# Optimization experiments

Measured on AMD Instinct MI355X. Metric: run time of the kernel, lower is better.

## Reference

```python
import jax, jax.numpy as jnp
import numpy as np

B, N, F_IN, F_OUT, H = 8, 1024, 128, 128, 8
D_K = F_OUT // H
NEG = -1.0e9


def setup_inputs() -> dict:
    key = jax.random.key(0)
    ks = jax.random.split(key, 10)
    X = jax.random.normal(ks[0], (B, N, F_IN), dtype=jnp.float32)
    A = (jax.random.uniform(ks[1], (B, N, N)) < 0.1).astype(jnp.float32)
    A = jnp.maximum(A, jnp.eye(N, dtype=jnp.float32)[None])
    s_in = 1.0 / np.sqrt(F_IN)
    s_out = 1.0 / np.sqrt(F_OUT)
    Wq = jax.random.uniform(ks[2], (F_OUT, F_IN), minval=-s_in, maxval=s_in)
    bq = jax.random.uniform(ks[3], (F_OUT,), minval=-s_in, maxval=s_in)
    Wk = jax.random.uniform(ks[4], (F_OUT, F_IN), minval=-s_in, maxval=s_in)
    bk = jax.random.uniform(ks[5], (F_OUT,), minval=-s_in, maxval=s_in)
    Wv = jax.random.uniform(ks[6], (F_OUT, F_IN), minval=-s_in, maxval=s_in)
    bv = jax.random.uniform(ks[7], (F_OUT,), minval=-s_in, maxval=s_in)
    Wo = jax.random.uniform(ks[8], (F_OUT, F_OUT), minval=-s_out, maxval=s_out)
    bo = jax.random.uniform(ks[9], (F_OUT,), minval=-s_out, maxval=s_out)
    return {"X": X, "A": A, "Wq": Wq, "bq": bq, "Wk": Wk, "bk": bk,
            "Wv": Wv, "bv": bv, "Wo": Wo, "bo": bo}


def reference(X, A, Wq, bq, Wk, bk, Wv, bv, Wo, bo):
    # QKV projections (nn.Linear: x @ W.T + b), split into heads
    Q = (X @ Wq.T + bq).reshape(B, N, H, D_K).transpose(0, 2, 1, 3)  # [B,H,N,d]
    K = (X @ Wk.T + bk).reshape(B, N, H, D_K).transpose(0, 2, 1, 3)
    V = (X @ Wv.T + bv).reshape(B, N, H, D_K).transpose(0, 2, 1, 3)
    scores = jnp.einsum('bhnd,bhmd->bhnm', Q, K) / jnp.sqrt(
        jnp.asarray(D_K, dtype=Q.dtype))
    # adjacency mask: entries with A<=0 set to -1e9 (matches masked_fill)
    scores = jnp.where(A[:, None, :, :] > 0, scores, NEG)
    attn = jax.nn.softmax(scores, axis=-1)  # dropout is identity at eval
    out = jnp.einsum('bhnm,bhmd->bhnd', attn, V)
    out = out.transpose(0, 2, 1, 3).reshape(B, N, H * D_K)
    return out @ Wo.T + bo
```

## Files before the change

### kernel.cpp

```cpp
#include <hip/hip_runtime.h>
#include <hip/hip_bf16.h>


#define BATCH 8
#define NNODE 1024
#define FEAT  128
#define NHEAD 8
#define CHUNKW 96
#define SPADW  100
#define MAXC   192

typedef __attribute__((ext_vector_type(8))) short short8v;
typedef __attribute__((ext_vector_type(4))) float float4v;

__device__ __forceinline__ unsigned short f2bf(float f) {
  union { float f; unsigned u; } c; c.f = f;
  unsigned u = c.u;
  u += 0x7fff + ((u >> 16) & 1);
  return (unsigned short)(u >> 16);
}
__device__ __forceinline__ float bf2f(unsigned short h) {
  union { unsigned u; float f; } c; c.u = ((unsigned)h) << 16;
  return c.f;
}


__global__ __launch_bounds__(256) void prep_kernel(
    const float* __restrict__ X, const float* __restrict__ A,
    const float* __restrict__ Wq, const float* __restrict__ Wk,
    const float* __restrict__ Wv, const float* __restrict__ Wo,
    unsigned short* __restrict__ Xh, unsigned short* __restrict__ Xl,
    unsigned short* __restrict__ Wh, unsigned short* __restrict__ Wl,
    float* __restrict__ WoT,
    unsigned short* __restrict__ AIdx, int* __restrict__ ACnt) {
  __shared__ unsigned short sIdxP[4][MAXC];
  const int bid = blockIdx.x;
  const int t = threadIdx.x;

  if (bid < 2048) {
    const int w = t >> 6;
    const int lane = t & 63;
    const int rowid = bid * 4 + w;
    const float* Arow = A + (size_t)rowid * NNODE;
    const unsigned long long lt = (1ull << lane) - 1ull;
    int cnt = 0;
    #pragma unroll
    for (int r = 0; r < 4; ++r) {
      const float4 av = *(const float4*)&Arow[r * 256 + lane * 4];
      const unsigned long long m0 = __ballot(av.x > 0.f);
      const unsigned long long m1 = __ballot(av.y > 0.f);
      const unsigned long long m2 = __ballot(av.z > 0.f);
      const unsigned long long m3 = __ballot(av.w > 0.f);
      const int c0n = __popcll(m0), c1n = __popcll(m1), c2n = __popcll(m2);
      const int j0 = r * 256 + lane * 4;
      if (av.x > 0.f) sIdxP[w][cnt + __popcll(m0 & lt)] = (unsigned short)j0;
      if (av.y > 0.f) sIdxP[w][cnt + c0n + __popcll(m1 & lt)] = (unsigned short)(j0 + 1);
      if (av.z > 0.f) sIdxP[w][cnt + c0n + c1n + __popcll(m2 & lt)] = (unsigned short)(j0 + 2);
      if (av.w > 0.f) sIdxP[w][cnt + c0n + c1n + c2n + __popcll(m3 & lt)] = (unsigned short)(j0 + 3);
      cnt += c0n + c1n + c2n + __popcll(m3);
    }
    for (int s = lane; s < cnt; s += 64)
      AIdx[(size_t)rowid * MAXC + s] = sIdxP[w][s];
    if (lane == 0) ACnt[rowid] = cnt;
  } else if (bid < 2560) {
    const int rb = bid - 2048;
    const int ks = t >> 6;
    const int lane = t & 63;
    const int r = rb * 16 + (lane & 15);
    const int k0 = ks * 32 + (lane >> 4) * 8;
    const float4 a = *(const float4*)&X[(size_t)r * 128 + k0];
    const float4 b = *(const float4*)&X[(size_t)r * 128 + k0 + 4];
    const float xs[8] = {a.x, a.y, a.z, a.w, b.x, b.y, b.z, b.w};
    short8v h8, l8;
    #pragma unroll
    for (int e = 0; e < 8; ++e) {
      const unsigned short hs = f2bf(xs[e]);
      h8[e] = (short)hs;
      l8[e] = (short)f2bf(xs[e] - bf2f(hs));
    }
    const size_t off = (((size_t)rb * 4 + ks) * 64 + lane) * 8;
    *(short8v*)&Xh[off] = h8;
    *(short8v*)&Xl[off] = l8;
  } else if (bid < 2584) {
    const int wb = bid - 2560;
    const int m = wb >> 3;
    const int p = wb & 7;
    const float* src = (m == 0) ? Wq : (m == 1) ? Wk : Wv;
    const int c = p * 16 + (t >> 4);
    const int k0 = (t & 15) * 8;
    const float4 a = *(const float4*)&src[c * 128 + k0];
    const float4 b = *(const float4*)&src[c * 128 + k0 + 4];
    const float xs[8] = {a.x, a.y, a.z, a.w, b.x, b.y, b.z, b.w};
    short8v h8, l8;
    #pragma unroll
    for (int e = 0; e < 8; ++e) {
      const unsigned short hs = f2bf(xs[e]);
      h8[e] = (short)hs;
      l8[e] = (short)f2bf(xs[e] - bf2f(hs));
    }
    const int ks = k0 >> 5;
    const int kg = (k0 >> 3) & 3;
    const int lanep = (c & 15) + 16 * kg;
    const size_t off = ((((size_t)m * 8 + p) * 4 + ks) * 64 + lanep) * 8;
    *(short8v*)&Wh[off] = h8;
    *(short8v*)&Wl[off] = l8;
  } else {
    const int c0 = (bid - 2584) * 8;
    #pragma unroll
    for (int e = 0; e < 4; ++e) {
      const int idx = t * 4 + e;
      const int cl = idx >> 7;
      const int k = idx & 127;
      WoT[(size_t)k * 128 + c0 + cl] = Wo[(size_t)(c0 + cl) * 128 + k];
    }
  }
}

__global__ __launch_bounds__(256) void qkv_mfma_kernel(
    const unsigned short* __restrict__ Xh, const unsigned short* __restrict__ Xl,
    const unsigned short* __restrict__ Wh, const unsigned short* __restrict__ Wl,
    const float* __restrict__ bq, const float* __restrict__ bk,
    const float* __restrict__ bv,
    unsigned short* __restrict__ Q, unsigned short* __restrict__ K,
    unsigned short* __restrict__ V) {
  const int w = threadIdx.x >> 6;
  const int l = threadIdx.x & 63;
  const int rb = blockIdx.x * 4 + w;
  const int ty = blockIdx.y;
  const int tz = blockIdx.z;
  const int c0 = ty * 32;
  const float* bias = (tz == 0) ? bq : (tz == 1) ? bk : bv;
  unsigned short* dst = (tz == 0) ? Q : (tz == 1) ? K : V;
  const float scale = (tz == 0) ? 0.25f : 1.0f;

  short8v aH[4], aL[4];
  #pragma unroll
  for (int ks = 0; ks < 4; ++ks) {
    const size_t ab = (((size_t)rb * 4 + ks) * 64 + l) * 8;
    aH[ks] = *(const short8v*)&Xh[ab];
    aL[ks] = *(const short8v*)&Xl[ab];
  }
  float4v acc[2] = {};
  const int wtile0 = tz * 8 + ty * 2;
  #pragma unroll
  for (int ks = 0; ks < 4; ++ks) {
    #pragma unroll
    for (int nt = 0; nt < 2; ++nt) {
      const size_t wb = ((((size_t)wtile0 + nt) * 4 + ks) * 64 + l) * 8;
      const short8v bh = *(const short8v*)&Wh[wb];
      const short8v bl = *(const short8v*)&Wl[wb];
      acc[nt] = __builtin_amdgcn_mfma_f32_16x16x32_bf16(aL[ks], bh, acc[nt], 0, 0, 0);
      acc[nt] = __builtin_amdgcn_mfma_f32_16x16x32_bf16(aH[ks], bl, acc[nt], 0, 0, 0);
      acc[nt] = __builtin_amdgcn_mfma_f32_16x16x32_bf16(aH[ks], bh, acc[nt], 0, 0, 0);
    }
  }

  const int row16 = l & 15;
  const int kgrp = l >> 4;
  #pragma unroll
  for (int nt = 0; nt < 2; ++nt) {
    const int col = c0 + nt * 16 + row16;
    const float bcol = bias[col];
    #pragma unroll
    for (int r = 0; r < 4; ++r) {
      const int row = rb * 16 + kgrp * 4 + r;
      dst[(size_t)row * 128 + col] = f2bf((acc[nt][r] + bcol) * scale);
    }
  }
}

__global__ __launch_bounds__(256) void attn_out_kernel(
    const unsigned short* __restrict__ Qb, const unsigned short* __restrict__ Kb,
    const unsigned short* __restrict__ Vb,
    const unsigned short* __restrict__ AIdx, const int* __restrict__ ACnt,
    const float* __restrict__ WoT, const float* __restrict__ bo,
    float* __restrict__ out) {
  __shared__ float sS[4][NHEAD][SPADW];
  __shared__ unsigned short sIdx[4][MAXC];
  __shared__ float sAx[2][2][64];
  __shared__ float sAy[2][2][64];
  __shared__ float sLh[2][2][NHEAD];
  __shared__ float sY[2][FEAT];

  const int t = threadIdx.x;
  const int w = t >> 6;
  const int lane = t & 63;
  const int pw = w >> 1;
  const int half = w & 1;
  const int b = blockIdx.x & 7;
  const int i0 = ((blockIdx.x >> 3) << 1);
  const int i = i0 + pw;
  const size_t bBase = (size_t)b * NNODE;
  const int rowid = (int)(bBase + i);
  const size_t rowQ = (size_t)rowid * FEAT;

  float q0, q1, q2, q3;
  {
    const ushort4 qu = *(const ushort4*)&Qb[rowQ + 4 * (lane & 31)];
    q0 = bf2f(qu.x); q1 = bf2f(qu.y); q2 = bf2f(qu.z); q3 = bf2f(qu.w);
  }

  const int cnt = ACnt[rowid];
  const int mid = (cnt + 1) >> 1;
  const int begin = half ? mid : 0;
  const int cw = (half ? cnt : mid) - begin;
  for (int s = lane; s < cw; s += 64)
    sIdx[w][s] = AIdx[(size_t)rowid * MAXC + begin + s];

  const int side = lane >> 5;
  const int sgrp = (lane & 31) >> 2;
  const int h = lane >> 3;
  float lacc = 0.f;
  float ax = 0.f, ay = 0.f;

  for (int c0 = 0; c0 < cw; c0 += CHUNKW) {
    const int cs = min(cw - c0, CHUNKW);

    for (int p2 = 0; p2 < cs; p2 += 2) {
      const int s = p2 + side;
      const bool valid = s < cs;
      const int j = sIdx[w][valid ? (c0 + s) : c0];
      const ushort4 ku = *(const ushort4*)&Kb[(bBase + j) * FEAT + 4 * (lane & 31)];
      float part = q0 * bf2f(ku.x) + q1 * bf2f(ku.y) +
                   q2 * bf2f(ku.z) + q3 * bf2f(ku.w);
      part += __shfl_xor(part, 1);
      part += __shfl_xor(part, 2);
      if (valid && (lane & 3) == 0) {
        const float p = __expf(part - 8.0f);
        sS[w][sgrp][s] = p;
        lacc += p;
      }
    }

    #pragma unroll 8
    for (int s = 0; s < cs; ++s) {
      const int j = sIdx[w][c0 + s];
      const unsigned vu = *(const unsigned*)&Vb[(bBase + j) * FEAT + 2 * lane];
      const float p = sS[w][h][s];
      ax += p * bf2f((unsigned short)(vu & 0xffff));
      ay += p * bf2f((unsigned short)(vu >> 16));
    }
  }

  const float lhv = __shfl(lacc, 4 * (lane & 7)) +
                    __shfl(lacc, 32 + 4 * (lane & 7));

  sAx[pw][half][lane] = ax;
  sAy[pw][half][lane] = ay;
  if (lane < NHEAD) sLh[pw][half][lane] = lhv;
  __syncthreads();

  if (half == 0) {
    const float axT = sAx[pw][0][lane] + sAx[pw][1][lane];
    const float ayT = sAy[pw][0][lane] + sAy[pw][1][lane];
    const float lT = sLh[pw][0][h] + sLh[pw][1][h];
    sY[pw][2 * lane] = axT / lT;
    sY[pw][2 * lane + 1] = ayT / lT;
  }
  __syncthreads();

  const int row = t >> 7;
  const int c = t & 127;
  const float* Yr = sY[row];
  float acc = bo[c];
  #pragma unroll 16
  for (int k = 0; k < FEAT; ++k)
    acc += Yr[k] * WoT[(size_t)k * 128 + c];
  out[(bBase + i0 + row) * FEAT + c] = acc;
}

extern "C" void kernel_launch(void* const* d_in, const int* in_sizes, int n_in,
                              void* d_out, int out_size, void* d_ws, size_t ws_size,
                              hipStream_t stream) {
  const float* X  = (const float*)d_in[0];
  const float* A  = (const float*)d_in[1];
  const float* Wq = (const float*)d_in[2];
  const float* bq = (const float*)d_in[3];
  const float* Wk = (const float*)d_in[4];
  const float* bk = (const float*)d_in[5];
  const float* Wv = (const float*)d_in[6];
  const float* bv = (const float*)d_in[7];
  const float* Wo = (const float*)d_in[8];
  const float* bo = (const float*)d_in[9];
  float* out = (float*)d_out;

  const size_t mat = (size_t)BATCH * NNODE * FEAT;
  unsigned short* Qd = (unsigned short*)d_ws;
  unsigned short* Kd = Qd + mat;
  unsigned short* Vd = Kd + mat;
  unsigned short* Xh = Vd + mat;
  unsigned short* Xl = Xh + mat;
  unsigned short* Wh = Xl + mat;
  unsigned short* Wl = Wh + 3 * 16384;
  unsigned short* AIdx = Wl + 3 * 16384;
  int* ACnt = (int*)(AIdx + (size_t)BATCH * NNODE * MAXC);
  float* WoT = (float*)(ACnt + BATCH * NNODE);

  hipLaunchKernelGGL(prep_kernel, dim3(2600), dim3(256), 0, stream,
                     X, A, Wq, Wk, Wv, Wo, Xh, Xl, Wh, Wl, WoT, AIdx, ACnt);
  hipLaunchKernelGGL(qkv_mfma_kernel, dim3(128, 4, 3), dim3(256), 0, stream,
                     Xh, Xl, Wh, Wl, bq, bk, bv, Qd, Kd, Vd);
  hipLaunchKernelGGL(attn_out_kernel, dim3(4096), dim3(256), 0, stream,
                     Qd, Kd, Vd, AIdx, ACnt, WoT, bo, out);
}
```

Baseline: 150.1 us.

## Fuse X bf16 hi/lo split into QKV kernel via shared memory

Removes the X split stage from the prep kernel and instead has the QKV MFMA kernel load fp32 X directly, split each value into bf16 high and low parts, and stage them in shared memory in MFMA fragment layout. Each block now covers 64 output columns instead of 32, so there are half as many blocks in y and each X tile is reused across four N-tiles. This avoids writing and re-reading the Xh/Xl workspace buffers. In exchange the split is recomputed by every (ty, tz) block, six times per row tile, and the scalar 2-byte shared-memory stores may cause bank conflicts.

```diff
diff --git a/kernel.cpp b/kernel.cpp
--- a/kernel.cpp
+++ b/kernel.cpp
@@ -26,10 +26,9 @@
 
 
 __global__ __launch_bounds__(256) void prep_kernel(
-    const float* __restrict__ X, const float* __restrict__ A,
+    const float* __restrict__ A,
     const float* __restrict__ Wq, const float* __restrict__ Wk,
     const float* __restrict__ Wv, const float* __restrict__ Wo,
-    unsigned short* __restrict__ Xh, unsigned short* __restrict__ Xl,
     unsigned short* __restrict__ Wh, unsigned short* __restrict__ Wl,
     float* __restrict__ WoT,
     unsigned short* __restrict__ AIdx, int* __restrict__ ACnt) {
@@ -62,27 +61,8 @@
     for (int s = lane; s < cnt; s += 64)
       AIdx[(size_t)rowid * MAXC + s] = sIdxP[w][s];
     if (lane == 0) ACnt[rowid] = cnt;
-  } else if (bid < 2560) {
-    const int rb = bid - 2048;
-    const int ks = t >> 6;
-    const int lane = t & 63;
-    const int r = rb * 16 + (lane & 15);
-    const int k0 = ks * 32 + (lane >> 4) * 8;
-    const float4 a = *(const float4*)&X[(size_t)r * 128 + k0];
-    const float4 b = *(const float4*)&X[(size_t)r * 128 + k0 + 4];
-    const float xs[8] = {a.x, a.y, a.z, a.w, b.x, b.y, b.z, b.w};
-    short8v h8, l8;
-    #pragma unroll
-    for (int e = 0; e < 8; ++e) {
-      const unsigned short hs = f2bf(xs[e]);
-      h8[e] = (short)hs;
-      l8[e] = (short)f2bf(xs[e] - bf2f(hs));
-    }
-    const size_t off = (((size_t)rb * 4 + ks) * 64 + lane) * 8;
-    *(short8v*)&Xh[off] = h8;
-    *(short8v*)&Xl[off] = l8;
-  } else if (bid < 2584) {
-    const int wb = bid - 2560;
+  } else if (bid < 2072) {
+    const int wb = bid - 2048;
     const int m = wb >> 3;
     const int p = wb & 7;
     const float* src = (m == 0) ? Wq : (m == 1) ? Wk : Wv;
@@ -105,7 +85,7 @@
     *(short8v*)&Wh[off] = h8;
     *(short8v*)&Wl[off] = l8;
   } else {
-    const int c0 = (bid - 2584) * 8;
+    const int c0 = (bid - 2072) * 8;
     #pragma unroll
     for (int e = 0; e < 4; ++e) {
       const int idx = t * 4 + e;
@@ -117,35 +97,62 @@
 }
 
 __global__ __launch_bounds__(256) void qkv_mfma_kernel(
-    const unsigned short* __restrict__ Xh, const unsigned short* __restrict__ Xl,
+    const float* __restrict__ X,
     const unsigned short* __restrict__ Wh, const unsigned short* __restrict__ Wl,
     const float* __restrict__ bq, const float* __restrict__ bk,
     const float* __restrict__ bv,
     unsigned short* __restrict__ Q, unsigned short* __restrict__ K,
     unsigned short* __restrict__ V) {
-  const int w = threadIdx.x >> 6;
-  const int l = threadIdx.x & 63;
-  const int rb = blockIdx.x * 4 + w;
+  __shared__ unsigned short sXh[4][4][64][8];
+  __shared__ unsigned short sXl[4][4][64][8];
+
+  const int t = threadIdx.x;
+  const int w = t >> 6;
+  const int l = t & 63;
+  const int r0 = blockIdx.x * 64;
   const int ty = blockIdx.y;
   const int tz = blockIdx.z;
-  const int c0 = ty * 32;
+  const int c0 = ty * 64;
   const float* bias = (tz == 0) ? bq : (tz == 1) ? bk : bv;
   unsigned short* dst = (tz == 0) ? Q : (tz == 1) ? K : V;
   const float scale = (tz == 0) ? 0.25f : 1.0f;
 
+  #pragma unroll
+  for (int it = 0; it < 8; ++it) {
+    const int idx = t + it * 256;
+    const int row = idx >> 5;
+    const int kq = (idx & 31) * 4;
+    const float4 xv = *(const float4*)&X[(size_t)(r0 + row) * 128 + kq];
+    const float xs[4] = {xv.x, xv.y, xv.z, xv.w};
+    const int rowgrp = row >> 4;
+    const int row16 = row & 15;
+    #pragma unroll
+    for (int e = 0; e < 4; ++e) {
+      const int k = kq + e;
+      const unsigned short hs = f2bf(xs[e]);
+      const unsigned short ls = f2bf(xs[e] - bf2f(hs));
+      const int ks = k >> 5;
+      const int lanep = row16 + 16 * ((k >> 3) & 3);
+      const int e7 = k & 7;
+      sXh[rowgrp][ks][lanep][e7] = hs;
+      sXl[rowgrp][ks][lanep][e7] = ls;
+    }
+  }
+  __syncthreads();
+
   short8v aH[4], aL[4];
   #pragma unroll
   for (int ks = 0; ks < 4; ++ks) {
-    const size_t ab = (((size_t)rb * 4 + ks) * 64 + l) * 8;
-    aH[ks] = *(const short8v*)&Xh[ab];
-    aL[ks] = *(const short8v*)&Xl[ab];
-  }
-  float4v acc[2] = {};
-  const int wtile0 = tz * 8 + ty * 2;
+    aH[ks] = *(const short8v*)&sXh[w][ks][l][0];
+    aL[ks] = *(const short8v*)&sXl[w][ks][l][0];
+  }
+
+  float4v acc[4] = {};
+  const int wtile0 = tz * 8 + ty * 4;
   #pragma unroll
   for (int ks = 0; ks < 4; ++ks) {
     #pragma unroll
-    for (int nt = 0; nt < 2; ++nt) {
+    for (int nt = 0; nt < 4; ++nt) {
       const size_t wb = ((((size_t)wtile0 + nt) * 4 + ks) * 64 + l) * 8;
       const short8v bh = *(const short8v*)&Wh[wb];
       const short8v bl = *(const short8v*)&Wl[wb];
@@ -158,12 +165,12 @@
   const int row16 = l & 15;
   const int kgrp = l >> 4;
   #pragma unroll
-  for (int nt = 0; nt < 2; ++nt) {
+  for (int nt = 0; nt < 4; ++nt) {
     const int col = c0 + nt * 16 + row16;
     const float bcol = bias[col];
     #pragma unroll
     for (int r = 0; r < 4; ++r) {
-      const int row = rb * 16 + kgrp * 4 + r;
+      const int row = r0 + w * 16 + kgrp * 4 + r;
       dst[(size_t)row * 128 + col] = f2bf((acc[nt][r] + bcol) * scale);
     }
   }
@@ -288,18 +295,16 @@
   unsigned short* Qd = (unsigned short*)d_ws;
   unsigned short* Kd = Qd + mat;
   unsigned short* Vd = Kd + mat;
-  unsigned short* Xh = Vd + mat;
-  unsigned short* Xl = Xh + mat;
-  unsigned short* Wh = Xl + mat;
+  unsigned short* Wh = Vd + mat;
   unsigned short* Wl = Wh + 3 * 16384;
   unsigned short* AIdx = Wl + 3 * 16384;
   int* ACnt = (int*)(AIdx + (size_t)BATCH * NNODE * MAXC);
   float* WoT = (float*)(ACnt + BATCH * NNODE);
 
-  hipLaunchKernelGGL(prep_kernel, dim3(2600), dim3(256), 0, stream,
-                     X, A, Wq, Wk, Wv, Wo, Xh, Xl, Wh, Wl, WoT, AIdx, ACnt);
-  hipLaunchKernelGGL(qkv_mfma_kernel, dim3(128, 4, 3), dim3(256), 0, stream,
-                     Xh, Xl, Wh, Wl, bq, bk, bv, Qd, Kd, Vd);
+  hipLaunchKernelGGL(prep_kernel, dim3(2088), dim3(256), 0, stream,
+                     A, Wq, Wk, Wv, Wo, Wh, Wl, WoT, AIdx, ACnt);
+  hipLaunchKernelGGL(qkv_mfma_kernel, dim3(128, 2, 3), dim3(256), 0, stream,
+                     X, Wh, Wl, bq, bk, bv, Qd, Kd, Vd);
   hipLaunchKernelGGL(attn_out_kernel, dim3(4096), dim3(256), 0, stream,
                      Qd, Kd, Vd, AIdx, ACnt, WoT, bo, out);
 }
```

Result: no change. 151.3 us (+0.8%).
